# Optimization experiments

Hardware: AMD Instinct MI355X
Metric: run time of the kernel (lower is better)

The kernel has to match this reference:

```python
import jax, jax.numpy as jnp
import numpy as np

N, M = 4096, 8192
NFEAT, EFEAT, NHID, NCLASS = 128, 64, 64, 16
ALPHA = 0.2
NEG = -9e15
BN_SCALE = np.float32(1.0 / np.sqrt(1.0 + 1e-5))  # eval BatchNorm: running stats (0,1), affine (1,0)


def _masked_att(hs, hd, a, mask):
    # hs: [P,F], hd: [Q,F], a: [2F], mask: [P,Q] binary
    F_ = hs.shape[1]
    logits = (hs @ a[:F_])[:, None] + (hd @ a[F_:])[None, :]            # [P,Q]
    logits = jnp.where(mask > 0, jax.nn.leaky_relu(logits, ALPHA), NEG)
    return jax.nn.softmax(logits, axis=1) @ hd                           # [P,F]


def _gat_layer(x, ex, adj, eadj, nem, Wn, We, ann, ane, aee, aen, concat):
    h = x @ Wn                                  # [N,F]
    g = ex @ We                                 # [M,F]
    Hn = _masked_att(h, h, ann, adj)            # node <- node neighbors
    He = _masked_att(h, g, ane, nem)            # node <- incident edges
    Ge = _masked_att(g, g, aee, eadj)           # edge <- adjacent edges
    Gn = _masked_att(g, h, aen, nem.T)          # edge <- endpoint nodes
    if concat:
        return (jax.nn.elu(jnp.concatenate([Hn, He], axis=1)),
                jax.nn.elu(jnp.concatenate([Ge, Gn], axis=1)))
    return Hn + He, Ge + Gn


def _mlp(h, W1, b1, W2, b2):
    h = jax.nn.relu((h @ W1 + b1) * BN_SCALE)
    return h @ W2 + b2


def _next_layer(h, A, W1, b1, W2, b2):
    pooled = A @ h                              # spmm(adj, h), dense-stored
    rep = _mlp(pooled, W1, b1, W2, b2)
    return jax.nn.relu(rep * BN_SCALE)


def setup_inputs() -> dict:
    key = jax.random.key(0)
    ks = jax.random.split(key, 40)
    f32 = jnp.float32
    x = jax.random.normal(ks[0], (N, NFEAT), f32)
    e_x = jax.random.normal(ks[1], (M, EFEAT), f32)
    adj = jnp.minimum((jax.random.uniform(ks[2], (N, N)) < 16.0 / N).astype(f32) + jnp.eye(N, dtype=f32), 1.0)
    e_adj = jnp.minimum((jax.random.uniform(ks[3], (M, M)) < 16.0 / M).astype(f32) + jnp.eye(M, dtype=f32), 1.0)
    n_e_adj = (jax.random.uniform(ks[4], (N, M)) < 4.0 / M).astype(f32)

    def lin(k, i, o):
        return jax.random.normal(k, (i, o), f32) * np.float32(1.0 / np.sqrt(i))

    def avec(k, F_):
        return jax.random.normal(k, (2 * F_,), f32) * np.float32(0.1)

    d = dict(x=x, e_x=e_x, adj=adj, e_adj=e_adj, n_e_adj=n_e_adj)
    # layer dims: (node_in, edge_in, out)
    dims = [(NFEAT, EFEAT, NHID), (2 * NHID, 2 * NHID, 2 * NHID), (64, 64, NCLASS)]
    ki = 5
    for li, (ni, ei, fo) in enumerate(dims):
        d[f'l{li}_Wn'] = lin(ks[ki], ni, fo); ki += 1
        d[f'l{li}_We'] = lin(ks[ki], ei, fo); ki += 1
        for nm in ('ann', 'ane', 'aee', 'aen'):
            d[f'l{li}_{nm}'] = avec(ks[ki], fo); ki += 1
    mdims = [(256, 64, 64), (64, 64, 64)]
    for mi, (i_, h_, o_) in enumerate(mdims):
        d[f'm{mi}_W1'] = lin(ks[ki], i_, h_); ki += 1
        d[f'm{mi}_b1'] = jnp.zeros((h_,), f32)
        d[f'm{mi}_W2'] = lin(ks[ki], h_, o_); ki += 1
        d[f'm{mi}_b2'] = jnp.zeros((o_,), f32)
    return d


def reference(x, e_x, adj, e_adj, n_e_adj,
              l0_Wn, l0_We, l0_ann, l0_ane, l0_aee, l0_aen,
              l1_Wn, l1_We, l1_ann, l1_ane, l1_aee, l1_aen,
              l2_Wn, l2_We, l2_ann, l2_ane, l2_aee, l2_aen,
              m0_W1, m0_b1, m0_W2, m0_b2,
              m1_W1, m1_b1, m1_W2, m1_b2):
    # dropout is identity in eval mode
    h, g = _gat_layer(x, e_x, adj, e_adj, n_e_adj, l0_Wn, l0_We, l0_ann, l0_ane, l0_aee, l0_aen, True)
    h, g = _gat_layer(h, g, adj, e_adj, n_e_adj, l1_Wn, l1_We, l1_ann, l1_ane, l1_aee, l1_aen, True)
    h_n, h_e = h, g
    h_n = _next_layer(h_n, adj, m0_W1, m0_b1, m0_W2, m0_b2)
    h_n = _next_layer(h_n, adj, m1_W1, m1_b1, m1_W2, m1_b2)
    h_e = _next_layer(h_e, e_adj, m0_W1, m0_b1, m0_W2, m0_b2)
    h_e = _next_layer(h_e, e_adj, m1_W1, m1_b1, m1_W2, m1_b2)
    fn, fe = _gat_layer(h_n, h_e, adj, e_adj, n_e_adj, l2_Wn, l2_We, l2_ann, l2_ane, l2_aee, l2_aen, False)
    return (jax.nn.log_softmax(jax.nn.elu(fn), axis=1),
            jax.nn.log_softmax(jax.nn.elu(fe), axis=1))
```

## Files before the change

### kernel.cpp

```cpp
#include <hip/hip_runtime.h>
#include <cmath>

constexpr int N_ = 4096;
constexpr int M_ = 8192;
constexpr float ALPHA_ = 0.2f;
constexpr float BN_SC = 0.9999950000374998f;
constexpr int CAP = 64;

typedef unsigned long long u64;
typedef unsigned short u16;

__device__ __forceinline__ float lrelu(float x) { return x > 0.f ? x : ALPHA_ * x; }
__device__ __forceinline__ float elu(float x) { return x > 0.f ? x : __expf(x) - 1.f; }

__device__ void pack_body(const float* __restrict__ m, u64* __restrict__ bits, int nw16) {
  int stride = 2048 * 512;
  u16* out = reinterpret_cast<u16*>(bits);
  for (int w = blockIdx.x * 512 + threadIdx.x; w < nw16; w += stride) {
    const float4* p = reinterpret_cast<const float4*>(m) + (size_t)w * 4;
    float4 v0 = p[0], v1 = p[1], v2 = p[2], v3 = p[3];
    unsigned mk =
        (v0.x > 0.5f ? 1u : 0u)      | (v0.y > 0.5f ? 2u : 0u)      |
        (v0.z > 0.5f ? 4u : 0u)      | (v0.w > 0.5f ? 8u : 0u)      |
        (v1.x > 0.5f ? 16u : 0u)     | (v1.y > 0.5f ? 32u : 0u)     |
        (v1.z > 0.5f ? 64u : 0u)     | (v1.w > 0.5f ? 128u : 0u)    |
        (v2.x > 0.5f ? 256u : 0u)    | (v2.y > 0.5f ? 512u : 0u)    |
        (v2.z > 0.5f ? 1024u : 0u)   | (v2.w > 0.5f ? 2048u : 0u)   |
        (v3.x > 0.5f ? 4096u : 0u)   | (v3.y > 0.5f ? 8192u : 0u)   |
        (v3.z > 0.5f ? 16384u : 0u)  | (v3.w > 0.5f ? 32768u : 0u);
    out[w] = (u16)mk;
  }
}

__global__ __launch_bounds__(256) void csr_bits(
    const u64* __restrict__ bA, const u64* __restrict__ bE, const u64* __restrict__ bN,
    int* __restrict__ cA, int* __restrict__ iA,
    int* __restrict__ cE, int* __restrict__ iE,
    int* __restrict__ cN, int* __restrict__ iN,
    int* __restrict__ cT, int* __restrict__ iT) {
  int wid = blockIdx.x * 4 + (threadIdx.x >> 6);
  int lane = threadIdx.x & 63;
  const u64* bits; int row, Qw; int* cnt; int* idx; bool tr = false;
  if (wid < N_)           { bits = bA; row = wid;            Qw = N_ / 64; cnt = cA; idx = iA; }
  else if (wid < N_ + M_) { bits = bE; row = wid - N_;       Qw = M_ / 64; cnt = cE; idx = iE; }
  else                    { bits = bN; row = wid - N_ - M_;  Qw = M_ / 64; cnt = cN; idx = iN; tr = true; }
  const u64* br = bits + (size_t)row * Qw;
  int total = 0;
  for (int w0 = 0; w0 < Qw; w0 += 64) {
    u64 b = br[w0 + lane];
    int c = __popcll(b);
    int pre = c;
#pragma unroll
    for (int t = 1; t < 64; t <<= 1) {
      int o = __shfl_up(pre, t);
      if (lane >= t) pre += o;
    }
    int base = total + pre - c;
    int jbase = (w0 + lane) * 64;
    while (b) {
      int bit = __ffsll(b) - 1;
      b &= b - 1;
      int j = jbase + bit;
      if (base < CAP) idx[(size_t)row * CAP + base] = j;
      if (tr) {
        int tp = atomicAdd(&cT[j], 1);
        if (tp < CAP) iT[(size_t)j * CAP + tp] = row;
      }
      base++;
    }
    total += __shfl(pre, 63);
  }
  if (lane == 0) cnt[row] = min(total, CAP);
}

struct PDOp {
  const float* X; const float* W; int K, P;
  const float* a0; const float* a1; const float* a2; const float* a3;
  float* o0; float* o1; float* o2; float* o3;
  float* Y;
};

template <int F>
__device__ void proj_body(const PDOp& op, float* part) {
  constexpr int RPB = 512 / F;
  constexpr int KC = 8192 / F;
  __shared__ float Wl[8192];
  __shared__ float dred[8][4];
  int rl = threadIdx.x / F;
  int f = threadIdx.x % F;
  int p = blockIdx.x * RPB + rl;
  bool act = p < op.P;
  float acc = 0.f;
  for (int k0 = 0; k0 < op.K; k0 += KC) {
    int kc = min(KC, op.K - k0);
    __syncthreads();
    for (int i = threadIdx.x; i < kc * F; i += 512) Wl[i] = op.W[(size_t)k0 * F + i];
    __syncthreads();
    if (act) {
      const float4* xr4 = reinterpret_cast<const float4*>(op.X + (size_t)p * op.K + k0);
      for (int k = 0; k < kc; k += 4) {
        float4 xv = xr4[k >> 2];
        acc = fmaf(xv.x, Wl[k * F + f], acc);
        acc = fmaf(xv.y, Wl[(k + 1) * F + f], acc);
        acc = fmaf(xv.z, Wl[(k + 2) * F + f], acc);
        acc = fmaf(xv.w, Wl[(k + 3) * F + f], acc);
      }
    }
  }
  if (act) op.Y[(size_t)p * F + f] = acc;
  float q0 = acc * op.a0[f];
  float q1 = acc * op.a1[f];
  float q2 = acc * op.a2[f];
  float q3 = acc * op.a3[f];
  constexpr int WID = F < 64 ? F : 64;
#pragma unroll
  for (int t = 1; t < WID; t <<= 1) {
    q0 += __shfl_xor(q0, t, WID);
    q1 += __shfl_xor(q1, t, WID);
    q2 += __shfl_xor(q2, t, WID);
    q3 += __shfl_xor(q3, t, WID);
  }
  if constexpr (F == 128) {
    int w = threadIdx.x >> 6;
    if ((threadIdx.x & 63) == 0) { dred[w][0] = q0; dred[w][1] = q1; dred[w][2] = q2; dred[w][3] = q3; }
    __syncthreads();
    if (act && f == 0) {
      int w0 = rl * 2;
      op.o0[p] = dred[w0][0] + dred[w0 + 1][0];
      op.o1[p] = dred[w0][1] + dred[w0 + 1][1];
      op.o2[p] = dred[w0][2] + dred[w0 + 1][2];
      op.o3[p] = dred[w0][3] + dred[w0 + 1][3];
    }
  } else {
    if (act && f == 0) { op.o0[p] = q0; op.o1[p] = q1; op.o2[p] = q2; op.o3[p] = q3; }
  }
  float* sred = Wl;
  __syncthreads();
  sred[rl * F + f] = act ? acc : 0.f;
  __syncthreads();
  if (rl == 0) {
    float s = 0.f;
    for (int r = 0; r < RPB; r++) s += sred[r * F + f];
    part[(size_t)blockIdx.x * F + f] = s;
  }
}

__global__ __launch_bounds__(512) void phase0(
    const float* adj, const float* eadj, const float* nem,
    u64* bA, u64* bE, u64* bN,
    PDOp A, PDOp B, float* partH, float* partG) {
  if (blockIdx.y == 0) {
    pack_body(adj, bA, N_ * N_ / 16);
    pack_body(eadj, bE, M_ * M_ / 16);
    pack_body(nem, bN, N_ * M_ / 16);
    return;
  }
  if (blockIdx.x >= 1024) return;
  if (blockIdx.y == 1) proj_body<64>(A, partH);
  else                 proj_body<64>(B, partG);
}

template <int F>
__global__ __launch_bounds__(512) void proj_l(PDOp A, PDOp B, float* partH, float* partG) {
  if (blockIdx.y == 0) proj_body<F>(A, partH);
  else                 proj_body<F>(B, partG);
}

template <int F>
__global__ __launch_bounds__(1024) void part_reduce(const float* __restrict__ partH,
                                                    const float* __restrict__ partG,
                                                    int nb,
                                                    float* __restrict__ oh, float* __restrict__ og) {
  constexpr int SL = 1024 / F;
  const float* part = blockIdx.y ? partG : partH;
  float* o = blockIdx.y ? og : oh;
  int f = threadIdx.x % F;
  int w = threadIdx.x / F;
  float s = 0.f;
  int b = w;
  for (; b + 8 * SL <= nb; b += 8 * SL) {
    float v0 = part[(size_t)(b + 0 * SL) * F + f];
    float v1 = part[(size_t)(b + 1 * SL) * F + f];
    float v2 = part[(size_t)(b + 2 * SL) * F + f];
    float v3 = part[(size_t)(b + 3 * SL) * F + f];
    float v4 = part[(size_t)(b + 4 * SL) * F + f];
    float v5 = part[(size_t)(b + 5 * SL) * F + f];
    float v6 = part[(size_t)(b + 6 * SL) * F + f];
    float v7 = part[(size_t)(b + 7 * SL) * F + f];
    s += ((v0 + v1) + (v2 + v3)) + ((v4 + v5) + (v6 + v7));
  }
  for (; b < nb; b += SL) s += part[(size_t)b * F + f];
  __shared__ float red[1024];
  red[threadIdx.x] = s;
  __syncthreads();
  if (w == 0) {
    float t = 0.f;
#pragma unroll
    for (int ww = 0; ww < SL; ww++) t += red[ww * F + f];
    o[f] = t;
  }
}

struct AOp {
  const int* cnt; int* idx; const float* s; const float* d;
  const float* Hd; const float* cs; float* out; int ldo, ocol, P, Q;
  int sortL; int* cTw;
};

template <int F>
__global__ __launch_bounds__(256) void att4(AOp A0, AOp A1, AOp A2, AOp A3) {
  int y = blockIdx.y;
  AOp op = y == 0 ? A0 : y == 1 ? A1 : y == 2 ? A2 : A3;
  constexpr int C = F / 64;
  int row = blockIdx.x * 4 + (threadIdx.x >> 6);
  int lane = threadIdx.x & 63;
  if (row >= op.P) return;
  int n = min(op.cnt[row], CAP);
  float acc[C];
  if (n == 0) {
    float invQ = 1.f / (float)op.Q;
#pragma unroll
    for (int c = 0; c < C; c++) acc[c] = op.cs[lane + c * 64] * invQ;
  } else {
    float sp = op.s[row];
    int* ip = op.idx + (size_t)row * CAP;
    int jl;
    if (op.sortL) {
      int v = lane < n ? ip[lane] : 0x7fffffff;
#pragma unroll
      for (int k = 2; k <= 64; k <<= 1) {
#pragma unroll
        for (int s = k >> 1; s > 0; s >>= 1) {
          int o = __shfl_xor(v, s);
          bool keepmin = (((lane & s) == 0) == ((lane & k) == 0));
          v = keepmin ? min(v, o) : max(v, o);
        }
      }
      if (lane < n) ip[lane] = v;
      if (lane == 0) op.cTw[row] = n;
      jl = lane < n ? v : 0;
    } else {
      jl = lane < n ? ip[lane] : 0;
    }
    float dl = lane < n ? op.d[jl] : -INFINITY;
    float mm = dl;
#pragma unroll
    for (int t = 1; t < 64; t <<= 1) mm = fmaxf(mm, __shfl_xor(mm, t));
    float m = lrelu(sp + mm);
    float el = lane < n ? __expf(lrelu(sp + dl) - m) : 0.f;
    float l = el;
#pragma unroll
    for (int t = 1; t < 64; t <<= 1) l += __shfl_xor(l, t);
    float invl = 1.f / l;
#pragma unroll
    for (int c = 0; c < C; c++) acc[c] = 0.f;
    int k = 0;
    for (; k + 2 <= n; k += 2) {
      int j0 = __shfl(jl, k), j1 = __shfl(jl, k + 1);
      float e0 = __shfl(el, k), e1 = __shfl(el, k + 1);
      const float* h0 = op.Hd + (size_t)j0 * F + lane;
      const float* h1 = op.Hd + (size_t)j1 * F + lane;
#pragma unroll
      for (int c = 0; c < C; c++) acc[c] = fmaf(e0, h0[c * 64], fmaf(e1, h1[c * 64], acc[c]));
    }
    if (k < n) {
      int j0 = __shfl(jl, k);
      float e0 = __shfl(el, k);
#pragma unroll
      for (int c = 0; c < C; c++) acc[c] = fmaf(e0, op.Hd[(size_t)j0 * F + lane + c * 64], acc[c]);
    }
#pragma unroll
    for (int c = 0; c < C; c++) acc[c] *= invl;
  }
  float* o = op.out + (size_t)row * op.ldo + op.ocol + lane;
#pragma unroll
  for (int c = 0; c < C; c++) o[c * 64] = elu(acc[c]);
}

template <int C>
__global__ __launch_bounds__(256) void nextlayer(
    const int* __restrict__ cA, const int* __restrict__ iA,
    const int* __restrict__ cE, const int* __restrict__ iE,
    const float* __restrict__ HdN, const float* __restrict__ HdM,
    const float* __restrict__ W1, const float* __restrict__ b1,
    const float* __restrict__ W2, const float* __restrict__ b2,
    float* __restrict__ outN, float* __restrict__ outM) {
  constexpr int KD = C * 64;
  int y = blockIdx.y;
  const int* cnt = y ? cE : cA;
  const int* idx = y ? iE : iA;
  const float* Hd = y ? HdM : HdN;
  float* out = y ? outM : outN;
  int P = y ? M_ : N_;
  int w = threadIdx.x >> 6, lane = threadIdx.x & 63;
  int row = blockIdx.x * 4 + w;
  if (row >= P) return;
  int n = min(cnt[row], CAP);
  const int* ip = idx + (size_t)row * CAP;
  int jl = lane < n ? ip[lane] : 0;
  float acc[C];
#pragma unroll
  for (int c = 0; c < C; c++) acc[c] = 0.f;
  int k = 0;
  for (; k + 2 <= n; k += 2) {
    int j0 = __shfl(jl, k), j1 = __shfl(jl, k + 1);
    const float* h0 = Hd + (size_t)j0 * KD + lane;
    const float* h1 = Hd + (size_t)j1 * KD + lane;
#pragma unroll
    for (int c = 0; c < C; c++) acc[c] += h0[c * 64] + h1[c * 64];
  }
  if (k < n) {
    int j0 = __shfl(jl, k);
#pragma unroll
    for (int c = 0; c < C; c++) acc[c] += Hd[(size_t)j0 * KD + lane + c * 64];
  }
  float y1 = 0.f;
#pragma unroll
  for (int c = 0; c < C; c++) {
    for (int kk = 0; kk < 64; kk++)
      y1 = fmaf(__shfl(acc[c], kk), W1[(c * 64 + kk) * 64 + lane], y1);
  }
  y1 = fmaxf((y1 + b1[lane]) * BN_SC, 0.f);
  float y2 = 0.f;
  for (int kk = 0; kk < 64; kk++)
    y2 = fmaf(__shfl(y1, kk), W2[kk * 64 + lane], y2);
  out[(size_t)row * 64 + lane] = fmaxf((y2 + b2[lane]) * BN_SC, 0.f);
}

__device__ __forceinline__ float att_col16(const int* cnt, const int* idx, float sp,
                                           const float* d, const float* Hd,
                                           const float* cs, int Q, int row, int c) {
  int n = min(cnt[row], CAP);
  if (n == 0) return cs[c] / (float)Q;
  const int* ip = idx + (size_t)row * CAP;
  float mm = -INFINITY;
  for (int k0 = 0; k0 < n; k0 += 16) {
    int k = k0 + c;
    float dv = k < n ? d[ip[k]] : -INFINITY;
    mm = fmaxf(mm, dv);
  }
#pragma unroll
  for (int t = 1; t < 16; t <<= 1) mm = fmaxf(mm, __shfl_xor(mm, t, 16));
  float m = lrelu(sp + mm);
  float l = 0.f, a = 0.f;
  for (int k0 = 0; k0 < n; k0 += 16) {
    int k = k0 + c;
    int jx = k < n ? ip[k] : 0;
    float dv = k < n ? d[jx] : 0.f;
    float ex = k < n ? __expf(lrelu(sp + dv) - m) : 0.f;
    int kmax = min(16, n - k0);
    for (int kk = 0; kk < kmax; kk++) {
      float e = __shfl(ex, kk, 16);
      int j = __shfl(jx, kk, 16);
      l += e;
      a = fmaf(e, Hd[(size_t)j * 16 + c], a);
    }
  }
  return a / l;
}

__global__ __launch_bounds__(256) void att_final(
    const int* __restrict__ cA, const int* __restrict__ iA, const float* __restrict__ s0, const float* __restrict__ d0,
    const int* __restrict__ cN, const int* __restrict__ iN, const float* __restrict__ s1, const float* __restrict__ d1,
    const int* __restrict__ cE, const int* __restrict__ iE, const float* __restrict__ s2, const float* __restrict__ d2,
    const int* __restrict__ cT, const int* __restrict__ iT, const float* __restrict__ s3, const float* __restrict__ d3,
    const float* __restrict__ h2, const float* __restrict__ g2,
    const float* __restrict__ csh, const float* __restrict__ csg,
    float* __restrict__ out) {
  int y = blockIdx.y;
  int gid = blockIdx.x * 256 + threadIdx.x;
  int row = gid >> 4, c = gid & 15;
  float v; float* dst;
  if (y == 0) {
    if (row >= N_) return;
    v = att_col16(cA, iA, s0[row], d0, h2, csh, N_, row, c)
      + att_col16(cN, iN, s1[row], d1, g2, csg, M_, row, c);
    dst = out + (size_t)row * 16 + c;
  } else {
    if (row >= M_) return;
    v = att_col16(cE, iE, s2[row], d2, g2, csg, M_, row, c)
      + att_col16(cT, iT, s3[row], d3, h2, csh, N_, row, c);
    dst = out + (size_t)(N_ + row) * 16 + c;
  }
  v = elu(v);
  float mx = v;
#pragma unroll
  for (int t = 1; t < 16; t <<= 1) mx = fmaxf(mx, __shfl_xor(mx, t, 16));
  float ex = __expf(v - mx);
  float sm = ex;
#pragma unroll
  for (int t = 1; t < 16; t <<= 1) sm += __shfl_xor(sm, t, 16);
  *dst = v - mx - __logf(sm);
}

extern "C" void kernel_launch(void* const* d_in, const int* in_sizes, int n_in,
                              void* d_out, int out_size, void* d_ws, size_t ws_size,
                              hipStream_t stream) {
  (void)in_sizes; (void)n_in; (void)out_size; (void)ws_size;
  const float* x    = (const float*)d_in[0];
  const float* e_x  = (const float*)d_in[1];
  const float* adj  = (const float*)d_in[2];
  const float* eadj = (const float*)d_in[3];
  const float* nem  = (const float*)d_in[4];
  const float* l_Wn[3]  = {(const float*)d_in[5],  (const float*)d_in[11], (const float*)d_in[17]};
  const float* l_We[3]  = {(const float*)d_in[6],  (const float*)d_in[12], (const float*)d_in[18]};
  const float* l_ann[3] = {(const float*)d_in[7],  (const float*)d_in[13], (const float*)d_in[19]};
  const float* l_ane[3] = {(const float*)d_in[8],  (const float*)d_in[14], (const float*)d_in[20]};
  const float* l_aee[3] = {(const float*)d_in[9],  (const float*)d_in[15], (const float*)d_in[21]};
  const float* l_aen[3] = {(const float*)d_in[10], (const float*)d_in[16], (const float*)d_in[22]};
  const float* m_W1[2] = {(const float*)d_in[23], (const float*)d_in[27]};
  const float* m_b1[2] = {(const float*)d_in[24], (const float*)d_in[28]};
  const float* m_W2[2] = {(const float*)d_in[25], (const float*)d_in[29]};
  const float* m_b2[2] = {(const float*)d_in[26], (const float*)d_in[30]};
  float* outp = (float*)d_out;

  char* wsp = (char*)d_ws;
  size_t off = 0;
  auto alloc = [&](size_t bytes) -> void* {
    void* p = wsp + off;
    off += (bytes + 255) & ~(size_t)255;
    return p;
  };
  int* cT = (int*)alloc((size_t)M_ * 4);
  size_t zero_bytes = off;

  u64* bA = (u64*)alloc((size_t)N_ * (N_ / 64) * 8);
  u64* bE = (u64*)alloc((size_t)M_ * (M_ / 64) * 8);
  u64* bN = (u64*)alloc((size_t)N_ * (M_ / 64) * 8);

  float* bufH = (float*)alloc((size_t)2048 * 128 * 4);
  float* bufG = (float*)alloc((size_t)2048 * 128 * 4);
  float* csh = (float*)alloc(3 * 128 * 4);
  float* csg = (float*)alloc(3 * 128 * 4);

  int* cA = (int*)alloc((size_t)N_ * 4);
  int* cE = (int*)alloc((size_t)M_ * 4);
  int* cN = (int*)alloc((size_t)N_ * 4);
  int* iA = (int*)alloc((size_t)N_ * CAP * 4);
  int* iE = (int*)alloc((size_t)M_ * CAP * 4);
  int* iN = (int*)alloc((size_t)N_ * CAP * 4);
  int* iT = (int*)alloc((size_t)M_ * CAP * 4);

  float* ht  = (float*)alloc((size_t)N_ * 128 * 4);
  float* gt  = (float*)alloc((size_t)M_ * 128 * 4);
  float* hA  = (float*)alloc((size_t)N_ * 128 * 4);
  float* gA  = (float*)alloc((size_t)M_ * 128 * 4);
  float* hB  = (float*)alloc((size_t)N_ * 256 * 4);
  float* gB  = (float*)alloc((size_t)M_ * 256 * 4);
  float* h64a = (float*)alloc((size_t)N_ * 64 * 4);
  float* g64a = (float*)alloc((size_t)M_ * 64 * 4);
  float* h64b = (float*)alloc((size_t)N_ * 64 * 4);
  float* g64b = (float*)alloc((size_t)M_ * 64 * 4);
  float* h16 = (float*)alloc((size_t)N_ * 16 * 4);
  float* g16 = (float*)alloc((size_t)M_ * 16 * 4);
  float* s0N = (float*)alloc((size_t)N_ * 4);
  float* d0N = (float*)alloc((size_t)N_ * 4);
  float* s1N = (float*)alloc((size_t)N_ * 4);
  float* d3N = (float*)alloc((size_t)N_ * 4);
  float* d1M = (float*)alloc((size_t)M_ * 4);
  float* s2M = (float*)alloc((size_t)M_ * 4);
  float* d2M = (float*)alloc((size_t)M_ * 4);
  float* s3M = (float*)alloc((size_t)M_ * 4);

  dim3 B(256);
  hipMemsetAsync(wsp, 0, zero_bytes, stream);

  auto mkH = [&](int F, const float* Xh, int Kh, float* Yh, int li) {
    return PDOp{Xh, l_Wn[li], Kh, N_, l_ann[li], l_ann[li] + F, l_ane[li], l_aen[li] + F,
                s0N, d0N, s1N, d3N, Yh};
  };
  auto mkG = [&](int F, const float* Xg, int Kg, float* Yg, int li) {
    return PDOp{Xg, l_We[li], Kg, M_, l_ane[li] + F, l_aee[li], l_aee[li] + F, l_aen[li],
                d1M, s2M, d2M, s3M, Yg};
  };

  phase0<<<dim3(2048, 3), dim3(512), 0, stream>>>(
      adj, eadj, nem, bA, bE, bN,
      mkH(64, x, 128, ht, 0), mkG(64, e_x, 64, gt, 0), bufH, bufG);
  part_reduce<64><<<dim3(1, 2), dim3(1024), 0, stream>>>(bufH, bufG, 1024, csh + 0, csg + 0);

  csr_bits<<<dim3((2 * N_ + M_) / 4), B, 0, stream>>>(bA, bE, bN,
                                                      cA, iA, cE, iE, cN, iN, cT, iT);

  att4<64><<<dim3(M_ / 4, 4), B, 0, stream>>>(
      AOp{cA, iA, s0N, d0N, ht, csh + 0, hA, 128, 0, N_, N_, 0, nullptr},
      AOp{cN, iN, s1N, d1M, gt, csg + 0, hA, 128, 64, N_, M_, 0, nullptr},
      AOp{cE, iE, s2M, d2M, gt, csg + 0, gA, 128, 0, M_, M_, 0, nullptr},
      AOp{cT, iT, s3M, d3N, ht, csh + 0, gA, 128, 64, M_, N_, 1, cT});

  proj_l<128><<<dim3(2048, 2), dim3(512), 0, stream>>>(
      mkH(128, hA, 128, ht, 1), mkG(128, gA, 128, gt, 1), bufH, bufG);
  part_reduce<128><<<dim3(1, 2), dim3(1024), 0, stream>>>(bufH, bufG, 2048, csh + 128, csg + 128);
  att4<128><<<dim3(M_ / 4, 4), B, 0, stream>>>(
      AOp{cA, iA, s0N, d0N, ht, csh + 128, hB, 256, 0, N_, N_, 0, nullptr},
      AOp{cN, iN, s1N, d1M, gt, csg + 128, hB, 256, 128, N_, M_, 0, nullptr},
      AOp{cE, iE, s2M, d2M, gt, csg + 128, gB, 256, 0, M_, M_, 0, nullptr},
      AOp{cT, iT, s3M, d3N, ht, csh + 128, gB, 256, 128, M_, N_, 0, nullptr});

  nextlayer<4><<<dim3(M_ / 4, 2), B, 0, stream>>>(cA, iA, cE, iE, hB, gB,
      m_W1[0], m_b1[0], m_W2[0], m_b2[0], h64a, g64a);
  nextlayer<1><<<dim3(M_ / 4, 2), B, 0, stream>>>(cA, iA, cE, iE, h64a, g64a,
      m_W1[1], m_b1[1], m_W2[1], m_b2[1], h64b, g64b);

  proj_l<16><<<dim3(256, 2), dim3(512), 0, stream>>>(
      mkH(16, h64b, 64, h16, 2), mkG(16, g64b, 64, g16, 2), bufH, bufG);
  part_reduce<16><<<dim3(1, 2), dim3(1024), 0, stream>>>(bufH, bufG, 256, csh + 256, csg + 256);
  att_final<<<dim3(M_ * 16 / 256, 2), B, 0, stream>>>(
      cA, iA, s0N, d0N, cN, iN, s1N, d1M, cE, iE, s2M, d2M, cT, iT, s3M, d3N,
      h16, g16, csh + 256, csg + 256, outp);
}
```

Before: 327.0 us.

## Pack adjacency masks with wavefront ballots and split projection from packing kernel

Replaces the per-thread 16-float bit-packing loop with a wave-cooperative packer: each lane loads one float4, four ballots collect the comparison bits, and a bit-spread interleave rebuilds row-ordered 64-bit words, so loads are fully coalesced. The fused phase0 kernel that ran packing and layer-0 projection side by side is split into a standalone pack kernel followed by csr_bits and a separate projection launch. This is meant to speed up the bandwidth-bound read of roughly 400 MB of dense masks, but it gives up the overlap between packing and projection and adds a launch.

```diff
diff --git a/kernel.cpp b/kernel.cpp
--- a/kernel.cpp
+++ b/kernel.cpp
@@ -8,27 +8,48 @@
 constexpr int CAP = 64;
 
 typedef unsigned long long u64;
-typedef unsigned short u16;
 
 __device__ __forceinline__ float lrelu(float x) { return x > 0.f ? x : ALPHA_ * x; }
 __device__ __forceinline__ float elu(float x) { return x > 0.f ? x : __expf(x) - 1.f; }
 
-__device__ void pack_body(const float* __restrict__ m, u64* __restrict__ bits, int nw16) {
-  int stride = 2048 * 512;
-  u16* out = reinterpret_cast<u16*>(bits);
-  for (int w = blockIdx.x * 512 + threadIdx.x; w < nw16; w += stride) {
-    const float4* p = reinterpret_cast<const float4*>(m) + (size_t)w * 4;
-    float4 v0 = p[0], v1 = p[1], v2 = p[2], v3 = p[3];
-    unsigned mk =
-        (v0.x > 0.5f ? 1u : 0u)      | (v0.y > 0.5f ? 2u : 0u)      |
-        (v0.z > 0.5f ? 4u : 0u)      | (v0.w > 0.5f ? 8u : 0u)      |
-        (v1.x > 0.5f ? 16u : 0u)     | (v1.y > 0.5f ? 32u : 0u)     |
-        (v1.z > 0.5f ? 64u : 0u)     | (v1.w > 0.5f ? 128u : 0u)    |
-        (v2.x > 0.5f ? 256u : 0u)    | (v2.y > 0.5f ? 512u : 0u)    |
-        (v2.z > 0.5f ? 1024u : 0u)   | (v2.w > 0.5f ? 2048u : 0u)   |
-        (v3.x > 0.5f ? 4096u : 0u)   | (v3.y > 0.5f ? 8192u : 0u)   |
-        (v3.z > 0.5f ? 16384u : 0u)  | (v3.w > 0.5f ? 32768u : 0u);
-    out[w] = (u16)mk;
+__device__ __forceinline__ u64 spread4(u64 x) {
+  x = (x | (x << 24)) & 0x000000ff000000ffull;
+  x = (x | (x << 12)) & 0x000f000f000f000full;
+  x = (x | (x << 6))  & 0x0303030303030303ull;
+  x = (x | (x << 3))  & 0x1111111111111111ull;
+  return x;
+}
+
+constexpr int CA_ = N_ * N_ / 256;
+constexpr int CE_ = M_ * M_ / 256;
+constexpr int CN_ = N_ * M_ / 256;
+constexpr int CTOT_ = CA_ + CE_ + CN_;
+
+__global__ __launch_bounds__(256) void pack3(const float* __restrict__ adj,
+                                             const float* __restrict__ eadj,
+                                             const float* __restrict__ nem,
+                                             u64* __restrict__ bA, u64* __restrict__ bE,
+                                             u64* __restrict__ bN) {
+  int wv = blockIdx.x * 4 + (threadIdx.x >> 6);
+  int lane = threadIdx.x & 63;
+  for (int c = wv; c < CTOT_; c += 8192) {
+    const float* src; u64* dst; int cc = c;
+    if (cc < CA_)            { src = adj;  dst = bA; }
+    else if (cc < CA_ + CE_) { src = eadj; dst = bE; cc -= CA_; }
+    else                     { src = nem;  dst = bN; cc -= CA_ + CE_; }
+    float4 v = reinterpret_cast<const float4*>(src)[(size_t)cc * 64 + lane];
+    u64 b0 = __ballot(v.x > 0.5f);
+    u64 b1 = __ballot(v.y > 0.5f);
+    u64 b2 = __ballot(v.z > 0.5f);
+    u64 b3 = __ballot(v.w > 0.5f);
+    if (lane < 4) {
+      int sh = 16 * lane;
+      u64 w = spread4((b0 >> sh) & 0xFFFFull)
+            | (spread4((b1 >> sh) & 0xFFFFull) << 1)
+            | (spread4((b2 >> sh) & 0xFFFFull) << 2)
+            | (spread4((b3 >> sh) & 0xFFFFull) << 3);
+      dst[(size_t)cc * 4 + lane] = w;
+    }
   }
 }
 
@@ -145,21 +166,6 @@
   }
 }
 
-__global__ __launch_bounds__(512) void phase0(
-    const float* adj, const float* eadj, const float* nem,
-    u64* bA, u64* bE, u64* bN,
-    PDOp A, PDOp B, float* partH, float* partG) {
-  if (blockIdx.y == 0) {
-    pack_body(adj, bA, N_ * N_ / 16);
-    pack_body(eadj, bE, M_ * M_ / 16);
-    pack_body(nem, bN, N_ * M_ / 16);
-    return;
-  }
-  if (blockIdx.x >= 1024) return;
-  if (blockIdx.y == 1) proj_body<64>(A, partH);
-  else                 proj_body<64>(B, partG);
-}
-
 template <int F>
 __global__ __launch_bounds__(512) void proj_l(PDOp A, PDOp B, float* partH, float* partG) {
   if (blockIdx.y == 0) proj_body<F>(A, partH);
@@ -474,13 +480,13 @@
                 d1M, s2M, d2M, s3M, Yg};
   };
 
-  phase0<<<dim3(2048, 3), dim3(512), 0, stream>>>(
-      adj, eadj, nem, bA, bE, bN,
+  pack3<<<dim3(2048), B, 0, stream>>>(adj, eadj, nem, bA, bE, bN);
+  csr_bits<<<dim3((2 * N_ + M_) / 4), B, 0, stream>>>(bA, bE, bN,
+                                                      cA, iA, cE, iE, cN, iN, cT, iT);
+
+  proj_l<64><<<dim3(1024, 2), dim3(512), 0, stream>>>(
       mkH(64, x, 128, ht, 0), mkG(64, e_x, 64, gt, 0), bufH, bufG);
   part_reduce<64><<<dim3(1, 2), dim3(1024), 0, stream>>>(bufH, bufG, 1024, csh + 0, csg + 0);
-
-  csr_bits<<<dim3((2 * N_ + M_) / 4), B, 0, stream>>>(bA, bE, bN,
-                                                      cA, iA, cE, iE, cN, iN, cT, iT);
 
   att4<64><<<dim3(M_ / 4, 4), B, 0, stream>>>(
       AOp{cA, iA, s0N, d0N, ht, csh + 0, hA, 128, 0, N_, N_, 0, nullptr},
```

New measurement: 343.5 us. 5.1% more time.
